# Kernel optimization log

Hardware: AMD Instinct MI355X
Metric: run time of the kernel (lower is better)

Reference implementation:

```python
import jax, jax.numpy as jnp
import numpy as np

B, T, F, H1, H2 = 16384, 10, 500, 256, 100  # batch, seq_len, noise_dim/seq_len, LSTM units, GRU units


def setup_inputs() -> dict:
    key = jax.random.key(0)
    ks = jax.random.split(key, 10)
    s = 0.02  # small init so relu activations stay bounded over time steps
    return {
        "noise": jax.random.normal(ks[0], (B, T * F), dtype=jnp.float32),
        "Wx_lstm": jax.random.normal(ks[1], (F, 4 * H1), dtype=jnp.float32) * s,
        "Wh_lstm": jax.random.normal(ks[2], (H1, 4 * H1), dtype=jnp.float32) * s,
        "b_lstm": jnp.zeros((4 * H1,), dtype=jnp.float32),
        "Wx_gru": jax.random.normal(ks[3], (H1, 3 * H2), dtype=jnp.float32) * s,
        "Wh_gru": jax.random.normal(ks[4], (H2, 3 * H2), dtype=jnp.float32) * s,
        "b_in_gru": jnp.zeros((3 * H2,), dtype=jnp.float32),
        "b_rec_gru": jnp.zeros((3 * H2,), dtype=jnp.float32),
        "Wd": jax.random.normal(ks[5], (H2, T), dtype=jnp.float32) * s,
        "bd": jnp.zeros((T,), dtype=jnp.float32),
    }


def _lstm(x, Wx, Wh, b):
    # x: [T, B, F]; Keras LSTM with activation='relu', recurrent_activation='sigmoid'
    Bn = x.shape[1]
    H = Wh.shape[0]
    def step(carry, x_t):
        h, c = carry
        z = x_t @ Wx + h @ Wh + b  # [B, 4H]
        i, f, g, o = jnp.split(z, 4, axis=-1)  # Keras gate order: i, f, c, o
        i = jax.nn.sigmoid(i)
        f = jax.nn.sigmoid(f)
        g = jax.nn.relu(g)
        o = jax.nn.sigmoid(o)
        c = f * c + i * g
        h = o * jax.nn.relu(c)
        return (h, c), h
    h0 = jnp.zeros((Bn, H), dtype=x.dtype)
    (_, _), hs = jax.lax.scan(step, (h0, h0), x)
    return hs  # [T, B, H]


def _gru(x, Wx, Wh, b_in, b_rec):
    # x: [T, B, H1]; Keras GRU (reset_after=True) with activation='relu'
    Bn = x.shape[1]
    H = Wh.shape[0]
    def step(h, x_t):
        mx = x_t @ Wx + b_in    # [B, 3H]
        mh = h @ Wh + b_rec     # [B, 3H]
        xz, xr, xh = jnp.split(mx, 3, axis=-1)  # Keras gate order: z, r, h
        hz, hr, hh = jnp.split(mh, 3, axis=-1)
        z = jax.nn.sigmoid(xz + hz)
        r = jax.nn.sigmoid(xr + hr)
        hcand = jax.nn.relu(xh + r * hh)
        h = z * h + (1.0 - z) * hcand
        return h, None
    h0 = jnp.zeros((Bn, H), dtype=x.dtype)
    h_final, _ = jax.lax.scan(step, h0, x)
    return h_final  # [B, H]


def reference(noise, Wx_lstm, Wh_lstm, b_lstm, Wx_gru, Wh_gru, b_in_gru, b_rec_gru, Wd, bd):
    Fdim = Wx_lstm.shape[0]
    Tdim = noise.shape[1] // Fdim
    x = noise.reshape(noise.shape[0], Tdim, Fdim)      # Reshape((T, F))
    x = jnp.transpose(x, (1, 0, 2))                    # [T, B, F] for scan
    hs = _lstm(x, Wx_lstm, Wh_lstm, b_lstm)            # [T, B, 256]
    h = _gru(hs, Wx_gru, Wh_gru, b_in_gru, b_rec_gru)  # [B, 100]
    return jax.nn.relu(h @ Wd + bd)                    # [B, T]
```

## Files before the change

### kernel.cpp

```cpp
#include <hip/hip_runtime.h>

#define Bsz 16384
#define TT 10
#define FF 500
#define H1c 256
#define H2c 100

typedef _Float16 half8 __attribute__((ext_vector_type(8)));
typedef float floatx4 __attribute__((ext_vector_type(4)));

__device__ __forceinline__ float sigm(float x) { return 1.0f / (1.0f + __expf(-x)); }

#define GLOAD16(g, l) __builtin_amdgcn_global_load_lds( \
    (const __attribute__((address_space(1))) void*)(g), \
    (__attribute__((address_space(3))) void*)(l), 16, 0, 0)

__global__ __launch_bounds__(256)
void conv_all(const float* __restrict__ noise, _Float16* __restrict__ xc)
{
    const int idx = blockIdx.x * 256 + threadIdx.x;
    const int rb = idx >> 6;
    const int kc = (idx & 63) << 3;
    const int b = rb / 10;
    const int t = rb - b * 10;
    const float* src = noise + (size_t)rb * FF + kc;
    half8 v;
    if (kc + 8 <= FF) {
        float4 u0 = *(const float4*)src;
        float4 u1 = *(const float4*)(src + 4);
        v[0] = (_Float16)u0.x; v[1] = (_Float16)u0.y; v[2] = (_Float16)u0.z; v[3] = (_Float16)u0.w;
        v[4] = (_Float16)u1.x; v[5] = (_Float16)u1.y; v[6] = (_Float16)u1.z; v[7] = (_Float16)u1.w;
    } else {
        #pragma unroll
        for (int j = 0; j < 8; ++j)
            v[j] = (kc + j < FF) ? (_Float16)src[j] : (_Float16)0.f;
    }
    *(half8*)(xc + ((size_t)t * Bsz + b) * 512 + kc) = v;
}

__global__ __launch_bounds__(256)
void prep_lstm_w(const float* __restrict__ Wx, const float* __restrict__ Wh,
                 _Float16* __restrict__ WT)
{
    const int idx = blockIdx.x * 256 + threadIdx.x;
    const int np = idx / 768, k = idx % 768;
    const int A2 = np >> 8, B2 = (np >> 6) & 3, g = (np >> 4) & 3, u = np & 15;
    const int U = A2 * 64 + B2 * 16 + u;
    const int col = g * 256 + U;
    float v = 0.f;
    if (k < 512) { if (k < FF) v = Wx[(size_t)k * 1024 + col]; }
    else v = Wh[(size_t)(k - 512) * 1024 + col];
    WT[idx] = (_Float16)v;
}

__global__ __launch_bounds__(256)
void prep_gru_w(const float* __restrict__ Wxg, const float* __restrict__ Whg,
                _Float16* __restrict__ WT)
{
    const int idx = blockIdx.x * 256 + threadIdx.x;
    if (idx >= 384 * 384) return;
    const int np = idx / 384, k = idx % 384;
    const int nb = np / 96, rem = np % 96;
    const int wxx = rem / 48, g = (rem % 48) / 16, u = rem & 15;
    const int U = nb * 32 + wxx * 16 + u;
    float v = 0.f;
    if (U < H2c) {
        if (k < 256) v = Wxg[(size_t)k * 300 + g * H2c + U];
        else if (k - 256 < H2c) v = Whg[(size_t)(k - 256) * 300 + g * H2c + U];
    }
    WT[idx] = (_Float16)v;
}

__device__ __forceinline__
void lstm_tile(int bid, const _Float16* __restrict__ xct, const _Float16* __restrict__ WT,
               const float* __restrict__ bias,
               const _Float16* __restrict__ h_prev, const float* __restrict__ c_prev,
               _Float16* __restrict__ h_out, float* __restrict__ c_out,
               int first, _Float16* smem)
{
    _Float16* As = smem;
    _Float16* Bs = smem + 32768;

    const int tid = threadIdx.x;
    const int lane = tid & 63;
    const int w = tid >> 6;
    const int wy = w >> 2, wx = w & 3;
    const int swz = (bid & 7) * 32 + (bid >> 3);
    const int row0 = (swz >> 2) * 256;
    const int nb = swz & 3;

    const int fr = lane & 15;
    const int l4 = lane >> 4;
    const int sr8 = lane >> 3;
    const int qsrc = (((lane & 7) ^ (sr8 & 7)) << 3);

    floatx4 acc[8][4];
    #pragma unroll
    for (int a = 0; a < 8; ++a)
        #pragma unroll
        for (int b = 0; b < 4; ++b) acc[a][b] = (floatx4){0.f, 0.f, 0.f, 0.f};

    const int nkt = first ? 8 : 12;

    #pragma unroll
    for (int q = 0; q < 4; ++q) {
        const int r = q * 64 + w * 8;
        GLOAD16(xct + (size_t)(row0 + r + sr8) * 512 + qsrc, &As[r * 64]);
        GLOAD16(WT + (size_t)(nb * 256 + r + sr8) * 768 + qsrc, &Bs[r * 64]);
    }
    __syncthreads();

    for (int T = 0; T < nkt; ++T) {
        const int pbase = (T & 1) * 16384;
        const int sbase = pbase ^ 16384;
        const int kb2 = (T + 1) * 64;
        const bool do_stage = (T + 1 < nkt);
        const bool from_x = kb2 < 512;

        #pragma unroll
        for (int q = 0; q < 4; ++q) {
            const int mh = q >> 1, nh = q & 1;
            half8 af[4][2], bf[2][2];
            #pragma unroll
            for (int j = 0; j < 4; ++j) {
                const int row = wy * 128 + (mh * 4 + j) * 16 + fr;
                #pragma unroll
                for (int ks = 0; ks < 2; ++ks) {
                    const int ch = (ks * 4 + l4) ^ (fr & 7);
                    af[j][ks] = *(const half8*)&As[pbase + row * 64 + ch * 8];
                }
            }
            #pragma unroll
            for (int jn = 0; jn < 2; ++jn) {
                const int row = wx * 64 + (nh * 2 + jn) * 16 + fr;
                #pragma unroll
                for (int ks = 0; ks < 2; ++ks) {
                    const int ch = (ks * 4 + l4) ^ (fr & 7);
                    bf[jn][ks] = *(const half8*)&Bs[pbase + row * 64 + ch * 8];
                }
            }
            if (do_stage) {
                const int r = q * 64 + w * 8;
                if (from_x)
                    GLOAD16(xct + (size_t)(row0 + r + sr8) * 512 + kb2 + qsrc, &As[sbase + r * 64]);
                else
                    GLOAD16(h_prev + (size_t)(row0 + r + sr8) * 256 + (kb2 - 512) + qsrc, &As[sbase + r * 64]);
                GLOAD16(WT + (size_t)(nb * 256 + r + sr8) * 768 + kb2 + qsrc, &Bs[sbase + r * 64]);
            }
            __builtin_amdgcn_s_setprio(1);
            #pragma unroll
            for (int ks = 0; ks < 2; ++ks)
                #pragma unroll
                for (int j = 0; j < 4; ++j)
                    #pragma unroll
                    for (int jn = 0; jn < 2; ++jn)
                        acc[mh * 4 + j][nh * 2 + jn] = __builtin_amdgcn_mfma_f32_16x16x32_f16(
                            af[j][ks], bf[jn][ks], acc[mh * 4 + j][nh * 2 + jn], 0, 0, 0);
            __builtin_amdgcn_s_setprio(0);
            __builtin_amdgcn_sched_barrier(0);
        }
        __syncthreads();
    }

    const int U = nb * 64 + wx * 16 + fr;
    const float bi = bias[0 * 256 + U];
    const float bff = bias[1 * 256 + U];
    const float bg = bias[2 * 256 + U];
    const float bo = bias[3 * 256 + U];
    const int rbase = row0 + wy * 128 + l4 * 4;
    #pragma unroll
    for (int mi = 0; mi < 8; ++mi) {
        #pragma unroll
        for (int r = 0; r < 4; ++r) {
            const int row = rbase + mi * 16 + r;
            const float cp = first ? 0.f : c_prev[(size_t)row * 256 + U];
            const float zi = acc[mi][0][r] + bi;
            const float zf = acc[mi][1][r] + bff;
            const float zg = acc[mi][2][r] + bg;
            const float zo = acc[mi][3][r] + bo;
            const float ig = sigm(zi), fg = sigm(zf), og = sigm(zo);
            const float gg = fmaxf(zg, 0.f);
            const float cv = fg * cp + ig * gg;
            const float hv = og * fmaxf(cv, 0.f);
            c_out[(size_t)row * 256 + U] = cv;
            h_out[(size_t)row * 256 + U] = (_Float16)hv;
        }
    }
}

__device__ __forceinline__
void gru_tile(int bid, int first,
              const _Float16* __restrict__ h_r, const _Float16* __restrict__ g16_r,
              const float* __restrict__ gf_r,
              const _Float16* __restrict__ WTg,
              const float* __restrict__ b_in, const float* __restrict__ b_rec,
              float* __restrict__ gf_w, _Float16* __restrict__ g16_w, _Float16* smem)
{
    _Float16* As = smem;
    _Float16* Bs = smem + 4096;

    const int tid = threadIdx.x;
    const int lane = tid & 63;
    const int w = tid >> 6;
    const int wq = w >> 2;
    const int wn = w & 3;
    const int rb0 = bid * 64;
    const int fr = lane & 15;
    const int l4 = lane >> 4;
    const int sr8 = lane >> 3;
    const int qsrc = (((lane & 7) ^ sr8) << 3);

    floatx4 accA[2][6], accB[2][6];
    #pragma unroll
    for (int a = 0; a < 2; ++a)
        #pragma unroll
        for (int b = 0; b < 6; ++b) {
            accA[a][b] = (floatx4){0.f, 0.f, 0.f, 0.f};
            accB[a][b] = (floatx4){0.f, 0.f, 0.f, 0.f};
        }

    const int nkt = first ? 4 : 6;
    for (int kt = 0; kt < nkt; ++kt) {
        const int kb = kt * 64;
        {
            const int r = w * 8;
            if (kt < 4)
                GLOAD16(h_r + (size_t)(rb0 + r + sr8) * 256 + kb + qsrc, &As[r * 64]);
            else
                GLOAD16(g16_r + (size_t)(rb0 + r + sr8) * 128 + (kb - 256) + qsrc, &As[r * 64]);
        }
        #pragma unroll
        for (int q = 0; q < 6; ++q) {
            const int r = q * 64 + w * 8;
            GLOAD16(WTg + (size_t)(r + sr8) * 384 + kb + qsrc, &Bs[r * 64]);
        }
        __syncthreads();
        #pragma unroll
        for (int ks = 0; ks < 2; ++ks) {
            half8 af[2], bf[6];
            const int ch0 = (ks * 4 + l4) ^ (fr & 7);
            #pragma unroll
            for (int mf = 0; mf < 2; ++mf) {
                const int row = wq * 32 + mf * 16 + fr;
                af[mf] = *(const half8*)&As[row * 64 + ch0 * 8];
            }
            #pragma unroll
            for (int nf = 0; nf < 6; ++nf) {
                const int row = wn * 96 + nf * 16 + fr;
                bf[nf] = *(const half8*)&Bs[row * 64 + ch0 * 8];
            }
            if (kt < 4) {
                #pragma unroll
                for (int mf = 0; mf < 2; ++mf)
                    #pragma unroll
                    for (int nf = 0; nf < 6; ++nf)
                        accA[mf][nf] = __builtin_amdgcn_mfma_f32_16x16x32_f16(af[mf], bf[nf], accA[mf][nf], 0, 0, 0);
            } else {
                #pragma unroll
                for (int mf = 0; mf < 2; ++mf)
                    #pragma unroll
                    for (int nf = 0; nf < 6; ++nf)
                        accB[mf][nf] = __builtin_amdgcn_mfma_f32_16x16x32_f16(af[mf], bf[nf], accB[mf][nf], 0, 0, 0);
            }
        }
        __syncthreads();
    }

    #pragma unroll
    for (int mf = 0; mf < 2; ++mf) {
        #pragma unroll
        for (int wxx = 0; wxx < 2; ++wxx) {
            const int U = wn * 32 + wxx * 16 + fr;
            const bool uv = U < H2c;
            const float bzi = uv ? b_in[U] : 0.f;
            const float bri = uv ? b_in[H2c + U] : 0.f;
            const float bhi = uv ? b_in[2 * H2c + U] : 0.f;
            const float bzr = uv ? b_rec[U] : 0.f;
            const float brr = uv ? b_rec[H2c + U] : 0.f;
            const float bhr = uv ? b_rec[2 * H2c + U] : 0.f;
            const int nf0 = wxx * 3;
            #pragma unroll
            for (int r = 0; r < 4; ++r) {
                const int row = rb0 + wq * 32 + mf * 16 + l4 * 4 + r;
                const float gp = (!first && uv) ? gf_r[(size_t)row * H2c + U] : 0.f;
                const float mxz = accA[mf][nf0 + 0][r] + bzi;
                const float mxr = accA[mf][nf0 + 1][r] + bri;
                const float mxh = accA[mf][nf0 + 2][r] + bhi;
                const float mhz = accB[mf][nf0 + 0][r] + bzr;
                const float mhr = accB[mf][nf0 + 1][r] + brr;
                const float mhh = accB[mf][nf0 + 2][r] + bhr;
                const float z = sigm(mxz + mhz);
                const float rr = sigm(mxr + mhr);
                const float hc = fmaxf(mxh + rr * mhh, 0.f);
                const float g = z * gp + (1.f - z) * hc;
                if (uv) gf_w[(size_t)row * H2c + U] = g;
                g16_w[(size_t)row * 128 + U] = uv ? (_Float16)g : (_Float16)0.f;
            }
        }
    }
}

__device__ __forceinline__
void dense_tile(int bid, const float* __restrict__ hg, const float* __restrict__ Wd,
                const float* __restrict__ bd, float* __restrict__ out)
{
    const int tid = threadIdx.x;
    if (tid < 64) {
        const int row = bid * 64 + tid;
        float acc[TT];
        #pragma unroll
        for (int j = 0; j < TT; ++j) acc[j] = 0.f;
        const float* gr = hg + (size_t)row * H2c;
        for (int k = 0; k < H2c; ++k) {
            const float xv = gr[k];
            #pragma unroll
            for (int j = 0; j < TT; ++j) acc[j] += xv * Wd[k * TT + j];
        }
        #pragma unroll
        for (int j = 0; j < TT; ++j)
            out[(size_t)row * TT + j] = fmaxf(acc[j] + bd[j], 0.f);
    }
}

__global__ __launch_bounds__(512, 2)
void step_fused(const _Float16* __restrict__ xct, const _Float16* __restrict__ WTl,
                const float* __restrict__ b_l,
                const _Float16* __restrict__ h_prev, const float* __restrict__ c_prev,
                _Float16* __restrict__ h_out, float* __restrict__ c_out,
                const _Float16* __restrict__ WTg,
                const float* __restrict__ b_in, const float* __restrict__ b_rec,
                const _Float16* __restrict__ g16_r, const float* __restrict__ gf_r,
                float* __restrict__ gf_w, _Float16* __restrict__ g16_w,
                int lstm_first, int gru_on, int gru_first)
{
    extern __shared__ _Float16 smem[];
    const int bid = blockIdx.x;
    lstm_tile(bid, xct, WTl, b_l, h_prev, c_prev, h_out, c_out, lstm_first, smem);
    if (gru_on)
        gru_tile(bid, gru_first, h_prev, g16_r, gf_r, WTg, b_in, b_rec, gf_w, g16_w, smem);
}

__global__ __launch_bounds__(512, 2)
void gru512(const _Float16* __restrict__ h_r, const _Float16* __restrict__ g16_r,
            const float* __restrict__ gf_r,
            const _Float16* __restrict__ WTg,
            const float* __restrict__ b_in, const float* __restrict__ b_rec,
            float* __restrict__ gf_w, _Float16* __restrict__ g16_w, int first)
{
    __shared__ _Float16 smem[28672];
    gru_tile(blockIdx.x, first, h_r, g16_r, gf_r, WTg, b_in, b_rec, gf_w, g16_w, smem);
}

__global__ __launch_bounds__(512)
void dense_out512(const float* __restrict__ hg, const float* __restrict__ Wd,
                  const float* __restrict__ bd, float* __restrict__ out)
{
    dense_tile(blockIdx.x, hg, Wd, bd, out);
}

extern "C" void kernel_launch(void* const* d_in, const int* in_sizes, int n_in,
                              void* d_out, int out_size, void* d_ws, size_t ws_size,
                              hipStream_t stream)
{
    const float* noise  = (const float*)d_in[0];
    const float* Wx_l   = (const float*)d_in[1];
    const float* Wh_l   = (const float*)d_in[2];
    const float* b_l    = (const float*)d_in[3];
    const float* Wx_g   = (const float*)d_in[4];
    const float* Wh_g   = (const float*)d_in[5];
    const float* b_in   = (const float*)d_in[6];
    const float* b_rec  = (const float*)d_in[7];
    const float* Wd     = (const float*)d_in[8];
    const float* bd     = (const float*)d_in[9];
    float* outf = (float*)d_out;

    char* p = (char*)d_ws;
    auto alloc = [&](size_t bytes) {
        char* r = p;
        p += (bytes + 255) & ~(size_t)255;
        return r;
    };
    _Float16* WTl  = (_Float16*)alloc((size_t)1024 * 768 * 2);
    _Float16* WTg  = (_Float16*)alloc((size_t)384 * 384 * 2);
    _Float16* xc   = (_Float16*)alloc((size_t)Bsz * TT * 512 * 2);
    _Float16* h16A = (_Float16*)alloc((size_t)Bsz * 256 * 2);
    _Float16* h16B = (_Float16*)alloc((size_t)Bsz * 256 * 2);
    float*    cA   = (float*)alloc((size_t)Bsz * 256 * 4);
    float*    cB   = (float*)alloc((size_t)Bsz * 256 * 4);
    float*    gA   = (float*)alloc((size_t)Bsz * 100 * 4);
    float*    gB   = (float*)alloc((size_t)Bsz * 100 * 4);
    _Float16* g16A = (_Float16*)alloc((size_t)Bsz * 128 * 2);
    _Float16* g16B = (_Float16*)alloc((size_t)Bsz * 128 * 2);

    (void)hipFuncSetAttribute((const void*)step_fused,
                              hipFuncAttributeMaxDynamicSharedMemorySize, 131072);

    conv_all<<<Bsz * TT * 64 / 256, 256, 0, stream>>>(noise, xc);
    prep_lstm_w<<<1024 * 768 / 256, 256, 0, stream>>>(Wx_l, Wh_l, WTl);
    prep_gru_w<<<(384 * 384 + 255) / 256, 256, 0, stream>>>(Wx_g, Wh_g, WTg);

    _Float16* hb[2] = {h16A, h16B};
    float*    cb[2] = {cA, cB};
    float*    gf[2] = {gA, gB};
    _Float16* gh[2] = {g16A, g16B};

    for (int t = 0; t < TT; ++t) {
        const int wi = t & 1, ri = (t + 1) & 1;
        step_fused<<<256, 512, 131072, stream>>>(
            xc + (size_t)t * Bsz * 512, WTl, b_l,
            hb[ri], cb[ri], hb[wi], cb[wi],
            WTg, b_in, b_rec, gh[wi], gf[wi], gf[ri], gh[ri],
            t == 0 ? 1 : 0, t >= 1 ? 1 : 0, t == 1 ? 1 : 0);
    }
    gru512<<<256, 512, 0, stream>>>(hb[1], gh[0], gf[0], WTg, b_in, b_rec, gf[1], gh[1], 0);
    dense_out512<<<256, 512, 0, stream>>>(gf[1], Wd, bd, outf);
}
```

Measured before the change: 572.4 us.

## Switch LSTM GEMM to 4-stage K=32 pipeline with fine-grained vmcnt waits

Result: slower. 598.1 us (+4.5%).

```diff
diff --git a/kernel.cpp b/kernel.cpp
--- a/kernel.cpp
+++ b/kernel.cpp
@@ -91,8 +91,9 @@
 
     const int fr = lane & 15;
     const int l4 = lane >> 4;
-    const int sr8 = lane >> 3;
-    const int qsrc = (((lane & 7) ^ (sr8 & 7)) << 3);
+    const int sr = lane >> 2;
+    const int sch = (((lane & 3) ^ ((lane >> 2) & 3)) << 3);
+    const int rch = ((l4 ^ (fr & 3)) << 3);
 
     floatx4 acc[8][4];
     #pragma unroll
@@ -100,66 +101,52 @@
         #pragma unroll
         for (int b = 0; b < 4; ++b) acc[a][b] = (floatx4){0.f, 0.f, 0.f, 0.f};
 
-    const int nkt = first ? 8 : 12;
-
-    #pragma unroll
-    for (int q = 0; q < 4; ++q) {
-        const int r = q * 64 + w * 8;
-        GLOAD16(xct + (size_t)(row0 + r + sr8) * 512 + qsrc, &As[r * 64]);
-        GLOAD16(WT + (size_t)(nb * 256 + r + sr8) * 768 + qsrc, &Bs[r * 64]);
-    }
-    __syncthreads();
+    const int nkt = first ? 16 : 24;
+
+    auto STAGE = [&](int T) {
+        const int buf = (T & 3) * 8192;
+        const int kb = T * 32;
+        const bool fx = kb < 512;
+        #pragma unroll
+        for (int i = 0; i < 2; ++i) {
+            const int R = i * 128 + w * 16;
+            if (fx)
+                GLOAD16(xct + (size_t)(row0 + R + sr) * 512 + kb + sch, &As[buf + R * 32]);
+            else
+                GLOAD16(h_prev + (size_t)(row0 + R + sr) * 256 + (kb - 512) + sch, &As[buf + R * 32]);
+            GLOAD16(WT + (size_t)(nb * 256 + R + sr) * 768 + kb + sch, &Bs[buf + R * 32]);
+        }
+    };
+
+    STAGE(0); STAGE(1); STAGE(2);
 
     for (int T = 0; T < nkt; ++T) {
-        const int pbase = (T & 1) * 16384;
-        const int sbase = pbase ^ 16384;
-        const int kb2 = (T + 1) * 64;
-        const bool do_stage = (T + 1 < nkt);
-        const bool from_x = kb2 < 512;
-
-        #pragma unroll
-        for (int q = 0; q < 4; ++q) {
-            const int mh = q >> 1, nh = q & 1;
-            half8 af[4][2], bf[2][2];
+        const int rem = nkt - 1 - T;
+        if (rem >= 2)      asm volatile("s_waitcnt vmcnt(8)" ::: "memory");
+        else if (rem == 1) asm volatile("s_waitcnt vmcnt(4)" ::: "memory");
+        else               asm volatile("s_waitcnt vmcnt(0)" ::: "memory");
+        __builtin_amdgcn_s_barrier();
+        __builtin_amdgcn_sched_barrier(0);
+
+        if (T + 3 < nkt) STAGE(T + 3);
+
+        const int bufo = (T & 3) * 8192;
+        half8 af[8], bf[4];
+        #pragma unroll
+        for (int j = 0; j < 8; ++j)
+            af[j] = *(const half8*)&As[bufo + (wy * 128 + j * 16 + fr) * 32 + rch];
+        #pragma unroll
+        for (int n = 0; n < 4; ++n)
+            bf[n] = *(const half8*)&Bs[bufo + (wx * 64 + n * 16 + fr) * 32 + rch];
+
+        __builtin_amdgcn_s_setprio(1);
+        #pragma unroll
+        for (int j = 0; j < 8; ++j)
             #pragma unroll
-            for (int j = 0; j < 4; ++j) {
-                const int row = wy * 128 + (mh * 4 + j) * 16 + fr;
-                #pragma unroll
-                for (int ks = 0; ks < 2; ++ks) {
-                    const int ch = (ks * 4 + l4) ^ (fr & 7);
-                    af[j][ks] = *(const half8*)&As[pbase + row * 64 + ch * 8];
-                }
-            }
-            #pragma unroll
-            for (int jn = 0; jn < 2; ++jn) {
-                const int row = wx * 64 + (nh * 2 + jn) * 16 + fr;
-                #pragma unroll
-                for (int ks = 0; ks < 2; ++ks) {
-                    const int ch = (ks * 4 + l4) ^ (fr & 7);
-                    bf[jn][ks] = *(const half8*)&Bs[pbase + row * 64 + ch * 8];
-                }
-            }
-            if (do_stage) {
-                const int r = q * 64 + w * 8;
-                if (from_x)
-                    GLOAD16(xct + (size_t)(row0 + r + sr8) * 512 + kb2 + qsrc, &As[sbase + r * 64]);
-                else
-                    GLOAD16(h_prev + (size_t)(row0 + r + sr8) * 256 + (kb2 - 512) + qsrc, &As[sbase + r * 64]);
-                GLOAD16(WT + (size_t)(nb * 256 + r + sr8) * 768 + kb2 + qsrc, &Bs[sbase + r * 64]);
-            }
-            __builtin_amdgcn_s_setprio(1);
-            #pragma unroll
-            for (int ks = 0; ks < 2; ++ks)
-                #pragma unroll
-                for (int j = 0; j < 4; ++j)
-                    #pragma unroll
-                    for (int jn = 0; jn < 2; ++jn)
-                        acc[mh * 4 + j][nh * 2 + jn] = __builtin_amdgcn_mfma_f32_16x16x32_f16(
-                            af[j][ks], bf[jn][ks], acc[mh * 4 + j][nh * 2 + jn], 0, 0, 0);
-            __builtin_amdgcn_s_setprio(0);
-            __builtin_amdgcn_sched_barrier(0);
-        }
-        __syncthreads();
+            for (int n = 0; n < 4; ++n)
+                acc[j][n] = __builtin_amdgcn_mfma_f32_16x16x32_f16(af[j], bf[n], acc[j][n], 0, 0, 0);
+        __builtin_amdgcn_s_setprio(0);
+        __builtin_amdgcn_sched_barrier(0);
     }
 
     const int U = nb * 64 + wx * 16 + fr;
@@ -194,11 +181,9 @@
               const float* __restrict__ gf_r,
               const _Float16* __restrict__ WTg,
               const float* __restrict__ b_in, const float* __restrict__ b_rec,
-              float* __restrict__ gf_w, _Float16* __restrict__ g16_w, _Float16* smem)
-{
-    _Float16* As = smem;
-    _Float16* Bs = smem + 4096;
-
+              float* __restrict__ gf_w, _Float16* __restrict__ g16_w,
+              _Float16* As, _Float16* Bs)
+{
     const int tid = threadIdx.x;
     const int lane = tid & 63;
     const int w = tid >> 6;
@@ -337,7 +322,8 @@
     const int bid = blockIdx.x;
     lstm_tile(bid, xct, WTl, b_l, h_prev, c_prev, h_out, c_out, lstm_first, smem);
     if (gru_on)
-        gru_tile(bid, gru_first, h_prev, g16_r, gf_r, WTg, b_in, b_rec, gf_w, g16_w, smem);
+        gru_tile(bid, gru_first, h_prev, g16_r, gf_r, WTg, b_in, b_rec, gf_w, g16_w,
+                 smem, smem + 32768);
 }
 
 __global__ __launch_bounds__(512, 2)
@@ -348,7 +334,8 @@
             float* __restrict__ gf_w, _Float16* __restrict__ g16_w, int first)
 {
     __shared__ _Float16 smem[28672];
-    gru_tile(blockIdx.x, first, h_r, g16_r, gf_r, WTg, b_in, b_rec, gf_w, g16_w, smem);
+    gru_tile(blockIdx.x, first, h_r, g16_r, gf_r, WTg, b_in, b_rec, gf_w, g16_w,
+             smem, smem + 4096);
 }
 
 __global__ __launch_bounds__(512)
```

## Fold per-step input conversion into step kernel and fuse GRU tail with dense

Applied to the files above, without the earlier changes.

Measured after the change: 657.4 us. +14.8%, slower.

```diff
diff --git a/kernel.cpp b/kernel.cpp
--- a/kernel.cpp
+++ b/kernel.cpp
@@ -15,15 +15,13 @@
     (const __attribute__((address_space(1))) void*)(g), \
     (__attribute__((address_space(3))) void*)(l), 16, 0, 0)
 
-__global__ __launch_bounds__(256)
-void conv_all(const float* __restrict__ noise, _Float16* __restrict__ xc)
-{
-    const int idx = blockIdx.x * 256 + threadIdx.x;
-    const int rb = idx >> 6;
-    const int kc = (idx & 63) << 3;
-    const int b = rb / 10;
-    const int t = rb - b * 10;
-    const float* src = noise + (size_t)rb * FF + kc;
+__device__ __forceinline__
+void conv_chunks(const float* __restrict__ noise, _Float16* __restrict__ xc,
+                 int tp, int gidx)
+{
+    const int b = gidx >> 6;
+    const int kc = (gidx & 63) << 3;
+    const float* src = noise + (size_t)b * (TT * FF) + tp * FF + kc;
     half8 v;
     if (kc + 8 <= FF) {
         float4 u0 = *(const float4*)src;
@@ -35,7 +33,13 @@
         for (int j = 0; j < 8; ++j)
             v[j] = (kc + j < FF) ? (_Float16)src[j] : (_Float16)0.f;
     }
-    *(half8*)(xc + ((size_t)t * Bsz + b) * 512 + kc) = v;
+    *(half8*)(xc + ((size_t)tp * Bsz + b) * 512 + kc) = v;
+}
+
+__global__ __launch_bounds__(256)
+void conv_plane0(const float* __restrict__ noise, _Float16* __restrict__ xc)
+{
+    conv_chunks(noise, xc, 0, blockIdx.x * 256 + threadIdx.x);
 }
 
 __global__ __launch_bounds__(256)
@@ -194,11 +198,9 @@
               const float* __restrict__ gf_r,
               const _Float16* __restrict__ WTg,
               const float* __restrict__ b_in, const float* __restrict__ b_rec,
-              float* __restrict__ gf_w, _Float16* __restrict__ g16_w, _Float16* smem)
-{
-    _Float16* As = smem;
-    _Float16* Bs = smem + 4096;
-
+              float* __restrict__ gf_w, _Float16* __restrict__ g16_w,
+              _Float16* As, _Float16* Bs)
+{
     const int tid = threadIdx.x;
     const int lane = tid & 63;
     const int w = tid >> 6;
@@ -331,31 +333,37 @@
                 const float* __restrict__ b_in, const float* __restrict__ b_rec,
                 const _Float16* __restrict__ g16_r, const float* __restrict__ gf_r,
                 float* __restrict__ gf_w, _Float16* __restrict__ g16_w,
-                int lstm_first, int gru_on, int gru_first)
+                const float* __restrict__ noise, _Float16* __restrict__ xc_all,
+                int lstm_first, int gru_on, int gru_first, int conv_plane)
 {
     extern __shared__ _Float16 smem[];
     const int bid = blockIdx.x;
     lstm_tile(bid, xct, WTl, b_l, h_prev, c_prev, h_out, c_out, lstm_first, smem);
     if (gru_on)
-        gru_tile(bid, gru_first, h_prev, g16_r, gf_r, WTg, b_in, b_rec, gf_w, g16_w, smem);
+        gru_tile(bid, gru_first, h_prev, g16_r, gf_r, WTg, b_in, b_rec, gf_w, g16_w,
+                 smem, smem + 32768);
+    if (conv_plane > 0) {
+        const int base = bid * 512 + threadIdx.x;
+        #pragma unroll
+        for (int j = 0; j < 8; ++j)
+            conv_chunks(noise, xc_all, conv_plane, base + j * 131072);
+    }
 }
 
 __global__ __launch_bounds__(512, 2)
-void gru512(const _Float16* __restrict__ h_r, const _Float16* __restrict__ g16_r,
-            const float* __restrict__ gf_r,
-            const _Float16* __restrict__ WTg,
-            const float* __restrict__ b_in, const float* __restrict__ b_rec,
-            float* __restrict__ gf_w, _Float16* __restrict__ g16_w, int first)
+void gru_dense_tail(const _Float16* __restrict__ h_r, const _Float16* __restrict__ g16_r,
+                    const float* __restrict__ gf_r,
+                    const _Float16* __restrict__ WTg,
+                    const float* __restrict__ b_in, const float* __restrict__ b_rec,
+                    float* __restrict__ gf_w, _Float16* __restrict__ g16_w,
+                    const float* __restrict__ Wd, const float* __restrict__ bd,
+                    float* __restrict__ out)
 {
     __shared__ _Float16 smem[28672];
-    gru_tile(blockIdx.x, first, h_r, g16_r, gf_r, WTg, b_in, b_rec, gf_w, g16_w, smem);
-}
-
-__global__ __launch_bounds__(512)
-void dense_out512(const float* __restrict__ hg, const float* __restrict__ Wd,
-                  const float* __restrict__ bd, float* __restrict__ out)
-{
-    dense_tile(blockIdx.x, hg, Wd, bd, out);
+    gru_tile(blockIdx.x, 0, h_r, g16_r, gf_r, WTg, b_in, b_rec, gf_w, g16_w,
+             smem, smem + 4096);
+    __syncthreads();
+    dense_tile(blockIdx.x, gf_w, Wd, bd, out);
 }
 
 extern "C" void kernel_launch(void* const* d_in, const int* in_sizes, int n_in,
@@ -395,7 +403,7 @@
     (void)hipFuncSetAttribute((const void*)step_fused,
                               hipFuncAttributeMaxDynamicSharedMemorySize, 131072);
 
-    conv_all<<<Bsz * TT * 64 / 256, 256, 0, stream>>>(noise, xc);
+    conv_plane0<<<Bsz * 64 / 256, 256, 0, stream>>>(noise, xc);
     prep_lstm_w<<<1024 * 768 / 256, 256, 0, stream>>>(Wx_l, Wh_l, WTl);
     prep_gru_w<<<(384 * 384 + 255) / 256, 256, 0, stream>>>(Wx_g, Wh_g, WTg);
 
@@ -410,8 +418,10 @@
             xc + (size_t)t * Bsz * 512, WTl, b_l,
             hb[ri], cb[ri], hb[wi], cb[wi],
             WTg, b_in, b_rec, gh[wi], gf[wi], gf[ri], gh[ri],
-            t == 0 ? 1 : 0, t >= 1 ? 1 : 0, t == 1 ? 1 : 0);
-    }
-    gru512<<<256, 512, 0, stream>>>(hb[1], gh[0], gf[0], WTg, b_in, b_rec, gf[1], gh[1], 0);
-    dense_out512<<<256, 512, 0, stream>>>(gf[1], Wd, bd, outf);
-}
+            noise, xc,
+            t == 0 ? 1 : 0, t >= 1 ? 1 : 0, t == 1 ? 1 : 0,
+            t + 1 < TT ? t + 1 : 0);
+    }
+    gru_dense_tail<<<256, 512, 0, stream>>>(hb[1], gh[0], gf[0], WTg, b_in, b_rec,
+                                            gf[1], gh[1], Wd, bd, outf);
+}
```

## Drop fp32 GRU state, fuse final GRU with dense, remap LSTM tiles per XCD

Applied to the files above, without the earlier changes.

After: 570.1 us. No clear change (-0.4%).

```diff
diff --git a/kernel.cpp b/kernel.cpp
--- a/kernel.cpp
+++ b/kernel.cpp
@@ -85,9 +85,9 @@
     const int lane = tid & 63;
     const int w = tid >> 6;
     const int wy = w >> 2, wx = w & 3;
-    const int swz = (bid & 7) * 32 + (bid >> 3);
-    const int row0 = (swz >> 2) * 256;
-    const int nb = swz & 3;
+    const int xcd = bid & 7;
+    const int nb = xcd >> 1;
+    const int row0 = (((xcd & 1) << 5) + (bid >> 3)) * 256;
 
     const int fr = lane & 15;
     const int l4 = lane >> 4;
@@ -191,14 +191,11 @@
 __device__ __forceinline__
 void gru_tile(int bid, int first,
               const _Float16* __restrict__ h_r, const _Float16* __restrict__ g16_r,
-              const float* __restrict__ gf_r,
               const _Float16* __restrict__ WTg,
               const float* __restrict__ b_in, const float* __restrict__ b_rec,
-              float* __restrict__ gf_w, _Float16* __restrict__ g16_w, _Float16* smem)
-{
-    _Float16* As = smem;
-    _Float16* Bs = smem + 4096;
-
+              _Float16* __restrict__ g16_w,
+              _Float16* As, _Float16* Bs)
+{
     const int tid = threadIdx.x;
     const int lane = tid & 63;
     const int w = tid >> 6;
@@ -282,7 +279,7 @@
             #pragma unroll
             for (int r = 0; r < 4; ++r) {
                 const int row = rb0 + wq * 32 + mf * 16 + l4 * 4 + r;
-                const float gp = (!first && uv) ? gf_r[(size_t)row * H2c + U] : 0.f;
+                const float gp = (!first && uv) ? (float)g16_r[(size_t)row * 128 + U] : 0.f;
                 const float mxz = accA[mf][nf0 + 0][r] + bzi;
                 const float mxr = accA[mf][nf0 + 1][r] + bri;
                 const float mxh = accA[mf][nf0 + 2][r] + bhi;
@@ -293,7 +290,6 @@
                 const float rr = sigm(mxr + mhr);
                 const float hc = fmaxf(mxh + rr * mhh, 0.f);
                 const float g = z * gp + (1.f - z) * hc;
-                if (uv) gf_w[(size_t)row * H2c + U] = g;
                 g16_w[(size_t)row * 128 + U] = uv ? (_Float16)g : (_Float16)0.f;
             }
         }
@@ -301,7 +297,7 @@
 }
 
 __device__ __forceinline__
-void dense_tile(int bid, const float* __restrict__ hg, const float* __restrict__ Wd,
+void dense_tile(int bid, const _Float16* __restrict__ hg, const float* __restrict__ Wd,
                 const float* __restrict__ bd, float* __restrict__ out)
 {
     const int tid = threadIdx.x;
@@ -310,9 +306,9 @@
         float acc[TT];
         #pragma unroll
         for (int j = 0; j < TT; ++j) acc[j] = 0.f;
-        const float* gr = hg + (size_t)row * H2c;
+        const _Float16* gr = hg + (size_t)row * 128;
         for (int k = 0; k < H2c; ++k) {
-            const float xv = gr[k];
+            const float xv = (float)gr[k];
             #pragma unroll
             for (int j = 0; j < TT; ++j) acc[j] += xv * Wd[k * TT + j];
         }
@@ -329,33 +325,30 @@
                 _Float16* __restrict__ h_out, float* __restrict__ c_out,
                 const _Float16* __restrict__ WTg,
                 const float* __restrict__ b_in, const float* __restrict__ b_rec,
-                const _Float16* __restrict__ g16_r, const float* __restrict__ gf_r,
-                float* __restrict__ gf_w, _Float16* __restrict__ g16_w,
+                const _Float16* __restrict__ g16_r, _Float16* __restrict__ g16_w,
                 int lstm_first, int gru_on, int gru_first)
 {
     extern __shared__ _Float16 smem[];
     const int bid = blockIdx.x;
     lstm_tile(bid, xct, WTl, b_l, h_prev, c_prev, h_out, c_out, lstm_first, smem);
     if (gru_on)
-        gru_tile(bid, gru_first, h_prev, g16_r, gf_r, WTg, b_in, b_rec, gf_w, g16_w, smem);
+        gru_tile(bid, gru_first, h_prev, g16_r, WTg, b_in, b_rec, g16_w,
+                 smem, smem + 32768);
 }
 
 __global__ __launch_bounds__(512, 2)
-void gru512(const _Float16* __restrict__ h_r, const _Float16* __restrict__ g16_r,
-            const float* __restrict__ gf_r,
-            const _Float16* __restrict__ WTg,
-            const float* __restrict__ b_in, const float* __restrict__ b_rec,
-            float* __restrict__ gf_w, _Float16* __restrict__ g16_w, int first)
+void gru_dense_tail(const _Float16* __restrict__ h_r, const _Float16* __restrict__ g16_r,
+                    const _Float16* __restrict__ WTg,
+                    const float* __restrict__ b_in, const float* __restrict__ b_rec,
+                    _Float16* __restrict__ g16_w,
+                    const float* __restrict__ Wd, const float* __restrict__ bd,
+                    float* __restrict__ out)
 {
     __shared__ _Float16 smem[28672];
-    gru_tile(blockIdx.x, first, h_r, g16_r, gf_r, WTg, b_in, b_rec, gf_w, g16_w, smem);
-}
-
-__global__ __launch_bounds__(512)
-void dense_out512(const float* __restrict__ hg, const float* __restrict__ Wd,
-                  const float* __restrict__ bd, float* __restrict__ out)
-{
-    dense_tile(blockIdx.x, hg, Wd, bd, out);
+    gru_tile(blockIdx.x, 0, h_r, g16_r, WTg, b_in, b_rec, g16_w,
+             smem, smem + 4096);
+    __syncthreads();
+    dense_tile(blockIdx.x, g16_w, Wd, bd, out);
 }
 
 extern "C" void kernel_launch(void* const* d_in, const int* in_sizes, int n_in,
@@ -387,8 +380,6 @@
     _Float16* h16B = (_Float16*)alloc((size_t)Bsz * 256 * 2);
     float*    cA   = (float*)alloc((size_t)Bsz * 256 * 4);
     float*    cB   = (float*)alloc((size_t)Bsz * 256 * 4);
-    float*    gA   = (float*)alloc((size_t)Bsz * 100 * 4);
-    float*    gB   = (float*)alloc((size_t)Bsz * 100 * 4);
     _Float16* g16A = (_Float16*)alloc((size_t)Bsz * 128 * 2);
     _Float16* g16B = (_Float16*)alloc((size_t)Bsz * 128 * 2);
 
@@ -401,7 +392,6 @@
 
     _Float16* hb[2] = {h16A, h16B};
     float*    cb[2] = {cA, cB};
-    float*    gf[2] = {gA, gB};
     _Float16* gh[2] = {g16A, g16B};
 
     for (int t = 0; t < TT; ++t) {
@@ -409,9 +399,9 @@
         step_fused<<<256, 512, 131072, stream>>>(
             xc + (size_t)t * Bsz * 512, WTl, b_l,
             hb[ri], cb[ri], hb[wi], cb[wi],
-            WTg, b_in, b_rec, gh[wi], gf[wi], gf[ri], gh[ri],
+            WTg, b_in, b_rec, gh[wi], gh[ri],
             t == 0 ? 1 : 0, t >= 1 ? 1 : 0, t == 1 ? 1 : 0);
     }
-    gru512<<<256, 512, 0, stream>>>(hb[1], gh[0], gf[0], WTg, b_in, b_rec, gf[1], gh[1], 0);
-    dense_out512<<<256, 512, 0, stream>>>(gf[1], Wd, bd, outf);
-}
+    gru_dense_tail<<<256, 512, 0, stream>>>(hb[1], gh[0], WTg, b_in, b_rec,
+                                            gh[1], Wd, bd, outf);
+}
```
